# Performance work log

Hardware: AMD Instinct MI355X
Metric: run time of the kernel (lower is better)

Reference implementation:

```python
import jax, jax.numpy as jnp
import numpy as np

HEADS = 16
DIM_HEAD = 64
NONCAUSAL_ATTN_LEN = 64


def setup_inputs() -> dict:
    key = jax.random.key(0)
    k1, k2, k3 = jax.random.split(key, 3)
    b, n, d = 2, 2048, 1024
    inner = HEADS * DIM_HEAD
    x = jax.random.normal(k1, (b, n, d), dtype=jnp.float32)
    mask = jnp.ones((b, n), dtype=bool)
    w_qkv = jax.random.normal(k2, (d, 3 * inner), dtype=jnp.float32) * 0.02
    w_out = jax.random.normal(k3, (inner, d), dtype=jnp.float32) * 0.02
    b_out = jnp.zeros((d,), dtype=jnp.float32)
    return {"x": x, "mask": mask, "w_qkv": w_qkv, "w_out": w_out, "b_out": b_out}


def reference(x, mask, w_qkv, w_out, b_out):
    b, n, _ = x.shape
    h, dh = HEADS, DIM_HEAD
    scale = dh ** -0.5
    qkv = x @ w_qkv                                  # [b, n, 3*h*dh]
    q, k, v = jnp.split(qkv, 3, axis=-1)
    # 'b n (h d) -> b h n d'
    reshape = lambda t: t.reshape(b, n, h, dh).transpose(0, 2, 1, 3)
    q, k, v = reshape(q), reshape(k), reshape(v)
    dots = jnp.einsum('bhid,bhjd->bhij', q, k) * scale  # [b,h,n,n]
    neg = -jnp.finfo(dots.dtype).max
    # padding mask: attend only where both query and key positions are valid
    pm = mask[:, None, :, None] & mask[:, None, None, :]
    dots = jnp.where(~pm, neg, dots)
    # causal mask (strict upper triangle), with noncausal prefix block unmasked
    cm = jnp.triu(jnp.ones((n, n), dtype=bool), k=1)
    L = NONCAUSAL_ATTN_LEN
    if L > 1:
        cm = cm.at[:L, :L].set(False)
    dots = jnp.where(cm, neg, dots)
    attn = jax.nn.softmax(dots, axis=-1)
    out = jnp.einsum('bhij,bhjd->bhid', attn, v)     # [b,h,n,dh]
    out = out.transpose(0, 2, 1, 3).reshape(b, n, h * dh)  # 'b h n d -> b n (h d)'
    return out @ w_out + b_out
```

## Files before the change

### kernel.cpp

```cpp
#include <hip/hip_runtime.h>

typedef __bf16 bf16x8 __attribute__((ext_vector_type(8)));
typedef __bf16 bf16x4 __attribute__((ext_vector_type(4)));
typedef float  f32x4  __attribute__((ext_vector_type(4)));

#define SC2 0.18033688011112042f

__device__ __forceinline__ void gload16(const void* g, void* l) {
    __builtin_amdgcn_global_load_lds(
        (const __attribute__((address_space(1))) unsigned int*)g,
        (__attribute__((address_space(3))) unsigned int*)l, 16, 0, 0);
}

__global__ __launch_bounds__(256) void cast_f32_bf16_k(
    const float* __restrict__ in, __bf16* __restrict__ out, int n4)
{
    int i = blockIdx.x * blockDim.x + threadIdx.x;
    if (i < n4) {
        float4 v = ((const float4*)in)[i];
        bf16x4 o;
        o[0] = (__bf16)v.x; o[1] = (__bf16)v.y; o[2] = (__bf16)v.z; o[3] = (__bf16)v.w;
        ((bf16x4*)out)[i] = o;
    }
}

__global__ __launch_bounds__(1024) void transpose_cast_k(
    const float* __restrict__ in, __bf16* __restrict__ out, int R, int C)
{
    __shared__ float tile[32][33];
    int c0 = blockIdx.x * 32, r0 = blockIdx.y * 32;
    int tx = threadIdx.x, ty = threadIdx.y;
    tile[ty][tx] = in[(size_t)(r0 + ty) * C + (c0 + tx)];
    __syncthreads();
    out[(size_t)(c0 + ty) * R + (r0 + tx)] = (__bf16)tile[tx][ty];
}

template<int MODE>
__global__ __launch_bounds__(256) void gemm_bf16_k(
    const __bf16* __restrict__ A, const __bf16* __restrict__ Bt,
    void* __restrict__ Cout, const float* __restrict__ bias,
    int M, int N, int K)
{
    __shared__ __bf16 As[128 * 32];
    __shared__ __bf16 Bs[128 * 32];
    const int tid = threadIdx.x;
    const int m0 = blockIdx.x * 128, n0 = blockIdx.y * 128;
    const int wave = tid >> 6, lane = tid & 63;
    const int lr = lane & 15, lk = lane >> 4;

    const int row4 = lane >> 2;
    const int sg   = (lane & 3) ^ (row4 & 3);

    const int wm = (wave >> 1) * 64, wn = (wave & 1) * 64;

    f32x4 acc[4][4] = {};

    for (int k0 = 0; k0 < K; k0 += 32) {
#pragma unroll
        for (int c = 0; c < 2; ++c) {
            int row = c * 64 + wave * 16 + row4;
            gload16(A  + (size_t)(m0 + row) * K + k0 + sg * 8,
                    (char*)As + c * 4096 + wave * 1024);
            gload16(Bt + (size_t)(n0 + row) * K + k0 + sg * 8,
                    (char*)Bs + c * 4096 + wave * 1024);
        }
        __syncthreads();

        bf16x8 af[4], bfr[4];
#pragma unroll
        for (int i = 0; i < 4; ++i) {
            int row = wm + i * 16 + lr;
            af[i]  = *(const bf16x8*)((char*)As + row * 64 + ((lk ^ (row & 3)) << 4));
        }
#pragma unroll
        for (int j = 0; j < 4; ++j) {
            int row = wn + j * 16 + lr;
            bfr[j] = *(const bf16x8*)((char*)Bs + row * 64 + ((lk ^ (row & 3)) << 4));
        }
        __builtin_amdgcn_s_setprio(1);
#pragma unroll
        for (int i = 0; i < 4; ++i)
#pragma unroll
            for (int j = 0; j < 4; ++j)
                acc[i][j] = __builtin_amdgcn_mfma_f32_16x16x32_bf16(
                    af[i], bfr[j], acc[i][j], 0, 0, 0);
        __builtin_amdgcn_s_setprio(0);
        __syncthreads();
    }

#pragma unroll
    for (int i = 0; i < 4; ++i) {
#pragma unroll
        for (int j = 0; j < 4; ++j) {
            int row0 = m0 + wm + i * 16 + lk * 4;
            int col  = n0 + wn + j * 16 + lr;
            if (MODE == 0) {
                int which = col >> 10, rem = col & 1023;
                int h = rem >> 6, dh = rem & 63;
                int bb = row0 >> 11, nn0 = row0 & 2047;
                if (which == 2) {
                    bf16x4 o;
#pragma unroll
                    for (int r = 0; r < 4; ++r) o[r] = (__bf16)acc[i][j][r];
                    size_t off = (size_t)8388608 +
                                 (((size_t)bb * 16 + h) * 64 + dh) * 2048 + nn0;
                    *(bf16x4*)((__bf16*)Cout + off) = o;
                } else {
#pragma unroll
                    for (int r = 0; r < 4; ++r) {
                        size_t off = ((((size_t)which * 2 + bb) * 16 + h) * 2048
                                      + nn0 + r) * 64 + dh;
                        ((__bf16*)Cout)[off] = (__bf16)acc[i][j][r];
                    }
                }
            } else {
#pragma unroll
                for (int r = 0; r < 4; ++r)
                    ((float*)Cout)[(size_t)(row0 + r) * N + col] =
                        acc[i][j][r] + bias[col];
            }
        }
    }
}

__global__ __launch_bounds__(256) void flash_attn_k(
    const __bf16* __restrict__ qkv, __bf16* __restrict__ out)
{
    __shared__ __bf16 Ks[2][64 * 64];
    __shared__ __bf16 Vt[2][64 * 64];
    __shared__ __bf16 Ps[4 * 16 * 64];

    const int tid = threadIdx.x;
    const int g = blockIdx.x;
    const int xcd = g & 7, i = g >> 3;
    const int bh = xcd + 8 * (i & 3);
    const int qt = 31 - (i >> 2);
    const int b = bh >> 4, h = bh & 15;
    const int wave = tid >> 6, lane = tid & 63;
    const int lr = lane & 15, lk = lane >> 4;

    const size_t headoff = ((size_t)b * 16 + h) * 2048 * 64;
    const __bf16* Qp  = qkv + headoff;
    const __bf16* Kp  = qkv + (size_t)4194304 + headoff;
    const __bf16* Vtp = qkv + (size_t)8388608 + headoff;

    const int row8 = lane >> 3;
    const int sg   = (lane & 7) ^ row8;

    bf16x8 qf[2];
    {
        const __bf16* qa = Qp + (size_t)(qt * 64 + wave * 16 + lr) * 64 + lk * 8;
        qf[0] = *(const bf16x8*)(qa);
        qf[1] = *(const bf16x8*)(qa + 32);
    }

    float m = -1e30f, l = 0.f;
    f32x4 acc_o[4] = {};

    char* PsW = (char*)Ps + wave * 2048;

    auto stage = [&](int t, int bufi) {
        const int j0 = t * 64;
#pragma unroll
        for (int c = 0; c < 2; ++c) {
            int row = c * 32 + wave * 8 + row8;
            gload16(Kp + (size_t)(j0 + row) * 64 + sg * 8,
                    (char*)&Ks[bufi][0] + c * 4096 + wave * 1024);
            gload16(Vtp + (size_t)row * 2048 + j0 + sg * 8,
                    (char*)&Vt[bufi][0] + c * 4096 + wave * 1024);
        }
    };

    auto process = [&](int bufi, bool diag) {
        f32x4 sacc[4] = {};
        __builtin_amdgcn_s_setprio(1);
#pragma unroll
        for (int nf = 0; nf < 4; ++nf) {
            int arow = nf * 16 + lr;
#pragma unroll
            for (int ks = 0; ks < 2; ++ks) {
                int kb = (arow * 128 + (ks * 32 + lk * 8) * 2) ^ ((arow & 7) << 4);
                bf16x8 kf = *(const bf16x8*)((char*)&Ks[bufi][0] + kb);
                sacc[nf] = __builtin_amdgcn_mfma_f32_16x16x32_bf16(
                    kf, qf[ks], sacc[nf], 0, 0, 0);
            }
        }
        __builtin_amdgcn_s_setprio(0);
        if (diag) {
#pragma unroll
            for (int nf = 0; nf < 4; ++nf)
#pragma unroll
                for (int r = 0; r < 4; ++r)
                    if (nf * 16 + lk * 4 + r > wave * 16 + lr)
                        sacc[nf][r] = -1e30f;
        }
        float v = sacc[0][0];
#pragma unroll
        for (int nf = 0; nf < 4; ++nf)
#pragma unroll
            for (int r = 0; r < 4; ++r) v = fmaxf(v, sacc[nf][r]);
        v = fmaxf(v, __shfl_xor(v, 16));
        v = fmaxf(v, __shfl_xor(v, 32));
        float alpha = 1.f;
        bool resc = __any(v - m > 8.f);
        if (resc) {
            float mnew = fmaxf(m, v);
            alpha = exp2f((m - mnew) * SC2);
            m = mnew;
        }
        float rsum = 0.f;
#pragma unroll
        for (int nf = 0; nf < 4; ++nf) {
            bf16x4 o;
#pragma unroll
            for (int r = 0; r < 4; ++r) {
                float p = exp2f((sacc[nf][r] - m) * SC2);
                rsum += p;
                o[r] = (__bf16)p;
            }
            int pb = (lr * 128 + nf * 32 + lk * 8) ^ ((lr & 7) << 4);
            *(bf16x4*)(PsW + pb) = o;
        }
        rsum += __shfl_xor(rsum, 16);
        rsum += __shfl_xor(rsum, 32);
        l = l * alpha + rsum;
        if (resc) {
            float a_r[4];
#pragma unroll
            for (int r = 0; r < 4; ++r) a_r[r] = __shfl(alpha, lk * 4 + r);
#pragma unroll
            for (int nf = 0; nf < 4; ++nf)
#pragma unroll
                for (int r = 0; r < 4; ++r) acc_o[nf][r] *= a_r[r];
        }
        __builtin_amdgcn_s_setprio(1);
#pragma unroll
        for (int ks = 0; ks < 2; ++ks) {
            int pb = (lr * 128 + ks * 64 + lk * 16) ^ ((lr & 7) << 4);
            bf16x8 pa = *(const bf16x8*)(PsW + pb);
#pragma unroll
            for (int nf = 0; nf < 4; ++nf) {
                int d = nf * 16 + lr;
                int vb = (d * 128 + ks * 64 + lk * 16) ^ ((d & 7) << 4);
                bf16x8 vf = *(const bf16x8*)((char*)&Vt[bufi][0] + vb);
                acc_o[nf] = __builtin_amdgcn_mfma_f32_16x16x32_bf16(
                    pa, vf, acc_o[nf], 0, 0, 0);
            }
        }
        __builtin_amdgcn_s_setprio(0);
    };

    const int nt = qt + 1;
    stage(0, 0);
    for (int t = 0; t < nt; ++t) {
        __syncthreads();
        if (t + 1 < nt) stage(t + 1, (t + 1) & 1);
        process(t & 1, t == qt && qt > 0);
    }

    float l_row[4];
#pragma unroll
    for (int r = 0; r < 4; ++r) l_row[r] = __shfl(l, lk * 4 + r);
    const int rowbase = (b << 11) + qt * 64 + wave * 16 + lk * 4;
    const int colbase = h * 64 + lr;
#pragma unroll
    for (int nf = 0; nf < 4; ++nf)
#pragma unroll
        for (int r = 0; r < 4; ++r)
            out[(size_t)(rowbase + r) * 1024 + colbase + nf * 16] =
                (__bf16)(acc_o[nf][r] / l_row[r]);
}

extern "C" void kernel_launch(void* const* d_in, const int* in_sizes, int n_in,
                              void* d_out, int out_size, void* d_ws, size_t ws_size,
                              hipStream_t stream)
{
    const float* x     = (const float*)d_in[0];
    const float* w_qkv = (const float*)d_in[2];
    const float* w_out = (const float*)d_in[3];
    const float* b_out = (const float*)d_in[4];

    char* ws = (char*)d_ws;
    __bf16* xb    = (__bf16*)(ws);
    __bf16* wqkvT = (__bf16*)(ws + 8388608);
    __bf16* woutT = (__bf16*)(ws + 14680064);
    __bf16* qkvp  = (__bf16*)(ws + 16777216);
    __bf16* aout  = (__bf16*)(ws + 41943040);

    cast_f32_bf16_k<<<4096, 256, 0, stream>>>(x, xb, 1048576);
    transpose_cast_k<<<dim3(96, 32), dim3(32, 32), 0, stream>>>(w_qkv, wqkvT, 1024, 3072);
    transpose_cast_k<<<dim3(32, 32), dim3(32, 32), 0, stream>>>(w_out, woutT, 1024, 1024);

    gemm_bf16_k<0><<<dim3(32, 24), 256, 0, stream>>>(xb, wqkvT, (void*)qkvp, nullptr,
                                                     4096, 3072, 1024);
    flash_attn_k<<<1024, 256, 0, stream>>>(qkvp, aout);
    gemm_bf16_k<1><<<dim3(32, 8), 256, 0, stream>>>(aout, woutT, (void*)d_out, b_out,
                                                    4096, 1024, 1024);
}
```

Measured before the change: 125.8 us.

## Load K/V fragments directly from global memory instead of double-buffered LDS staging

Drops the shared-memory double buffers for K and V and the per-tile __syncthreads. Each wave now reads its MFMA operands straight from global memory, relying on L1/L2 to serve the redundant reads across the four waves. It also sets a launch-bounds occupancy hint of 6, rewrites the max reduction as a tree, and replaces the final division with a reciprocal multiply. The cost is higher global and L2 traffic, with each wave reading K/V separately and using strided V loads, plus exposed load latency now that there is no explicit prefetch.

```diff
diff --git a/kernel.cpp b/kernel.cpp
--- a/kernel.cpp
+++ b/kernel.cpp
@@ -123,29 +123,23 @@
     }
 }
 
-__global__ __launch_bounds__(256) void flash_attn_k(
+__global__ __launch_bounds__(256, 6) void flash_attn_k(
     const __bf16* __restrict__ qkv, __bf16* __restrict__ out)
 {
-    __shared__ __bf16 Ks[2][64 * 64];
-    __shared__ __bf16 Vt[2][64 * 64];
     __shared__ __bf16 Ps[4 * 16 * 64];
 
-    const int tid = threadIdx.x;
     const int g = blockIdx.x;
     const int xcd = g & 7, i = g >> 3;
     const int bh = xcd + 8 * (i & 3);
     const int qt = 31 - (i >> 2);
     const int b = bh >> 4, h = bh & 15;
-    const int wave = tid >> 6, lane = tid & 63;
+    const int wave = threadIdx.x >> 6, lane = threadIdx.x & 63;
     const int lr = lane & 15, lk = lane >> 4;
 
     const size_t headoff = ((size_t)b * 16 + h) * 2048 * 64;
     const __bf16* Qp  = qkv + headoff;
     const __bf16* Kp  = qkv + (size_t)4194304 + headoff;
     const __bf16* Vtp = qkv + (size_t)8388608 + headoff;
-
-    const int row8 = lane >> 3;
-    const int sg   = (lane & 7) ^ row8;
 
     bf16x8 qf[2];
     {
@@ -158,35 +152,28 @@
     f32x4 acc_o[4] = {};
 
     char* PsW = (char*)Ps + wave * 2048;
-
-    auto stage = [&](int t, int bufi) {
+    const __bf16* Kl = Kp  + lr * 64 + lk * 8;
+    const __bf16* Vl = Vtp + lr * 2048 + lk * 8;
+
+    for (int t = 0; t <= qt; ++t) {
         const int j0 = t * 64;
-#pragma unroll
-        for (int c = 0; c < 2; ++c) {
-            int row = c * 32 + wave * 8 + row8;
-            gload16(Kp + (size_t)(j0 + row) * 64 + sg * 8,
-                    (char*)&Ks[bufi][0] + c * 4096 + wave * 1024);
-            gload16(Vtp + (size_t)row * 2048 + j0 + sg * 8,
-                    (char*)&Vt[bufi][0] + c * 4096 + wave * 1024);
-        }
-    };
-
-    auto process = [&](int bufi, bool diag) {
+        const __bf16* Kt = Kl + j0 * 64;
+        const __bf16* Vt = Vl + j0;
+
         f32x4 sacc[4] = {};
         __builtin_amdgcn_s_setprio(1);
 #pragma unroll
         for (int nf = 0; nf < 4; ++nf) {
-            int arow = nf * 16 + lr;
 #pragma unroll
             for (int ks = 0; ks < 2; ++ks) {
-                int kb = (arow * 128 + (ks * 32 + lk * 8) * 2) ^ ((arow & 7) << 4);
-                bf16x8 kf = *(const bf16x8*)((char*)&Ks[bufi][0] + kb);
+                bf16x8 kf = *(const bf16x8*)(Kt + nf * 1024 + ks * 32);
                 sacc[nf] = __builtin_amdgcn_mfma_f32_16x16x32_bf16(
                     kf, qf[ks], sacc[nf], 0, 0, 0);
             }
         }
         __builtin_amdgcn_s_setprio(0);
-        if (diag) {
+
+        if (t == qt && qt > 0) {
 #pragma unroll
             for (int nf = 0; nf < 4; ++nf)
 #pragma unroll
@@ -194,13 +181,15 @@
                     if (nf * 16 + lk * 4 + r > wave * 16 + lr)
                         sacc[nf][r] = -1e30f;
         }
-        float v = sacc[0][0];
-#pragma unroll
-        for (int nf = 0; nf < 4; ++nf)
-#pragma unroll
-            for (int r = 0; r < 4; ++r) v = fmaxf(v, sacc[nf][r]);
+
+        float v = fmaxf(fmaxf(fmaxf(sacc[0][0], sacc[0][1]), fmaxf(sacc[0][2], sacc[0][3])),
+                        fmaxf(fmaxf(sacc[1][0], sacc[1][1]), fmaxf(sacc[1][2], sacc[1][3])));
+        float v2 = fmaxf(fmaxf(fmaxf(sacc[2][0], sacc[2][1]), fmaxf(sacc[2][2], sacc[2][3])),
+                         fmaxf(fmaxf(sacc[3][0], sacc[3][1]), fmaxf(sacc[3][2], sacc[3][3])));
+        v = fmaxf(v, v2);
         v = fmaxf(v, __shfl_xor(v, 16));
         v = fmaxf(v, __shfl_xor(v, 32));
+
         float alpha = 1.f;
         bool resc = __any(v - m > 8.f);
         if (resc) {
@@ -208,6 +197,7 @@
             alpha = exp2f((m - mnew) * SC2);
             m = mnew;
         }
+
         float rsum = 0.f;
 #pragma unroll
         for (int nf = 0; nf < 4; ++nf) {
@@ -233,6 +223,7 @@
 #pragma unroll
                 for (int r = 0; r < 4; ++r) acc_o[nf][r] *= a_r[r];
         }
+
         __builtin_amdgcn_s_setprio(1);
 #pragma unroll
         for (int ks = 0; ks < 2; ++ks) {
@@ -240,27 +231,17 @@
             bf16x8 pa = *(const bf16x8*)(PsW + pb);
 #pragma unroll
             for (int nf = 0; nf < 4; ++nf) {
-                int d = nf * 16 + lr;
-                int vb = (d * 128 + ks * 64 + lk * 16) ^ ((d & 7) << 4);
-                bf16x8 vf = *(const bf16x8*)((char*)&Vt[bufi][0] + vb);
+                bf16x8 vf = *(const bf16x8*)(Vt + nf * 32768 + ks * 32);
                 acc_o[nf] = __builtin_amdgcn_mfma_f32_16x16x32_bf16(
                     pa, vf, acc_o[nf], 0, 0, 0);
             }
         }
         __builtin_amdgcn_s_setprio(0);
-    };
-
-    const int nt = qt + 1;
-    stage(0, 0);
-    for (int t = 0; t < nt; ++t) {
-        __syncthreads();
-        if (t + 1 < nt) stage(t + 1, (t + 1) & 1);
-        process(t & 1, t == qt && qt > 0);
     }
 
     float l_row[4];
 #pragma unroll
-    for (int r = 0; r < 4; ++r) l_row[r] = __shfl(l, lk * 4 + r);
+    for (int r = 0; r < 4; ++r) l_row[r] = 1.f / __shfl(l, lk * 4 + r);
     const int rowbase = (b << 11) + qt * 64 + wave * 16 + lk * 4;
     const int colbase = h * 64 + lr;
 #pragma unroll
@@ -268,7 +249,7 @@
 #pragma unroll
         for (int r = 0; r < 4; ++r)
             out[(size_t)(rowbase + r) * 1024 + colbase + nf * 16] =
-                (__bf16)(acc_o[nf][r] / l_row[r]);
+                (__bf16)(acc_o[nf][r] * l_row[r]);
 }
 
 extern "C" void kernel_launch(void* const* d_in, const int* in_sizes, int n_in,
```

After: 223.7 us. +77.9%, slower.

## Pair causal query tiles per block and fold softmax scale into Q

Applied to the files above, without the earlier changes.

Each attention block now handles two query tiles, qt and 31-qt, from the same head. They share every staged K/V tile, which evens out causal work across blocks and halves the grid to 512. The QKV GEMM epilogue pre-multiplies Q by scale*log2(e), so the softmax exp2 no longer needs a multiply, and the final normalization uses a reciprocal instead of a divide. In exchange it holds two sets of Q fragments and accumulators, which raises register pressure, and Q is rounded to bf16 after scaling.

```diff
diff --git a/kernel.cpp b/kernel.cpp
--- a/kernel.cpp
+++ b/kernel.cpp
@@ -106,11 +106,12 @@
                                  (((size_t)bb * 16 + h) * 64 + dh) * 2048 + nn0;
                     *(bf16x4*)((__bf16*)Cout + off) = o;
                 } else {
+                    float sc = (which == 0) ? SC2 : 1.f;
 #pragma unroll
                     for (int r = 0; r < 4; ++r) {
                         size_t off = ((((size_t)which * 2 + bb) * 16 + h) * 2048
                                       + nn0 + r) * 64 + dh;
-                        ((__bf16*)Cout)[off] = (__bf16)acc[i][j][r];
+                        ((__bf16*)Cout)[off] = (__bf16)(acc[i][j][r] * sc);
                     }
                 }
             } else {
@@ -130,13 +131,13 @@
     __shared__ __bf16 Vt[2][64 * 64];
     __shared__ __bf16 Ps[4 * 16 * 64];
 
-    const int tid = threadIdx.x;
     const int g = blockIdx.x;
     const int xcd = g & 7, i = g >> 3;
     const int bh = xcd + 8 * (i & 3);
-    const int qt = 31 - (i >> 2);
+    const int qp = i >> 2;
+    const int qtA = qp, qtB = 31 - qp;
     const int b = bh >> 4, h = bh & 15;
-    const int wave = tid >> 6, lane = tid & 63;
+    const int wave = threadIdx.x >> 6, lane = threadIdx.x & 63;
     const int lr = lane & 15, lk = lane >> 4;
 
     const size_t headoff = ((size_t)b * 16 + h) * 2048 * 64;
@@ -147,15 +148,18 @@
     const int row8 = lane >> 3;
     const int sg   = (lane & 7) ^ row8;
 
-    bf16x8 qf[2];
+    bf16x8 qfA[2], qfB[2];
     {
-        const __bf16* qa = Qp + (size_t)(qt * 64 + wave * 16 + lr) * 64 + lk * 8;
-        qf[0] = *(const bf16x8*)(qa);
-        qf[1] = *(const bf16x8*)(qa + 32);
-    }
-
-    float m = -1e30f, l = 0.f;
-    f32x4 acc_o[4] = {};
+        const __bf16* qa = Qp + (size_t)(qtA * 64 + wave * 16 + lr) * 64 + lk * 8;
+        qfA[0] = *(const bf16x8*)(qa);
+        qfA[1] = *(const bf16x8*)(qa + 32);
+        const __bf16* qb = Qp + (size_t)(qtB * 64 + wave * 16 + lr) * 64 + lk * 8;
+        qfB[0] = *(const bf16x8*)(qb);
+        qfB[1] = *(const bf16x8*)(qb + 32);
+    }
+
+    float mA = -1e30f, lA = 0.f, mB = -1e30f, lB = 0.f;
+    f32x4 oA[4] = {}, oB[4] = {};
 
     char* PsW = (char*)Ps + wave * 2048;
 
@@ -171,7 +175,8 @@
         }
     };
 
-    auto process = [&](int bufi, bool diag) {
+    auto process = [&](int bufi, const bf16x8 (&qf)[2], float& m, float& l,
+                       f32x4 (&acc_o)[4], bool diag) {
         f32x4 sacc[4] = {};
         __builtin_amdgcn_s_setprio(1);
 #pragma unroll
@@ -194,18 +199,18 @@
                     if (nf * 16 + lk * 4 + r > wave * 16 + lr)
                         sacc[nf][r] = -1e30f;
         }
-        float v = sacc[0][0];
-#pragma unroll
-        for (int nf = 0; nf < 4; ++nf)
-#pragma unroll
-            for (int r = 0; r < 4; ++r) v = fmaxf(v, sacc[nf][r]);
+        float v = fmaxf(fmaxf(fmaxf(sacc[0][0], sacc[0][1]), fmaxf(sacc[0][2], sacc[0][3])),
+                        fmaxf(fmaxf(sacc[1][0], sacc[1][1]), fmaxf(sacc[1][2], sacc[1][3])));
+        float v2 = fmaxf(fmaxf(fmaxf(sacc[2][0], sacc[2][1]), fmaxf(sacc[2][2], sacc[2][3])),
+                         fmaxf(fmaxf(sacc[3][0], sacc[3][1]), fmaxf(sacc[3][2], sacc[3][3])));
+        v = fmaxf(v, v2);
         v = fmaxf(v, __shfl_xor(v, 16));
         v = fmaxf(v, __shfl_xor(v, 32));
         float alpha = 1.f;
         bool resc = __any(v - m > 8.f);
         if (resc) {
             float mnew = fmaxf(m, v);
-            alpha = exp2f((m - mnew) * SC2);
+            alpha = exp2f(m - mnew);
             m = mnew;
         }
         float rsum = 0.f;
@@ -214,7 +219,7 @@
             bf16x4 o;
 #pragma unroll
             for (int r = 0; r < 4; ++r) {
-                float p = exp2f((sacc[nf][r] - m) * SC2);
+                float p = exp2f(sacc[nf][r] - m);
                 rsum += p;
                 o[r] = (__bf16)p;
             }
@@ -250,25 +255,32 @@
         __builtin_amdgcn_s_setprio(0);
     };
 
-    const int nt = qt + 1;
+    const int nt = qtB + 1;
     stage(0, 0);
     for (int t = 0; t < nt; ++t) {
         __syncthreads();
         if (t + 1 < nt) stage(t + 1, (t + 1) & 1);
-        process(t & 1, t == qt && qt > 0);
-    }
-
-    float l_row[4];
-#pragma unroll
-    for (int r = 0; r < 4; ++r) l_row[r] = __shfl(l, lk * 4 + r);
-    const int rowbase = (b << 11) + qt * 64 + wave * 16 + lk * 4;
+        if (t <= qtA) process(t & 1, qfA, mA, lA, oA, t == qtA && qtA > 0);
+        process(t & 1, qfB, mB, lB, oB, t == qtB);
+    }
+
+    float lAr[4], lBr[4];
+#pragma unroll
+    for (int r = 0; r < 4; ++r) {
+        lAr[r] = 1.f / __shfl(lA, lk * 4 + r);
+        lBr[r] = 1.f / __shfl(lB, lk * 4 + r);
+    }
+    const int rowbase = (b << 11) + wave * 16 + lk * 4;
     const int colbase = h * 64 + lr;
 #pragma unroll
     for (int nf = 0; nf < 4; ++nf)
 #pragma unroll
-        for (int r = 0; r < 4; ++r)
-            out[(size_t)(rowbase + r) * 1024 + colbase + nf * 16] =
-                (__bf16)(acc_o[nf][r] / l_row[r]);
+        for (int r = 0; r < 4; ++r) {
+            out[(size_t)(rowbase + qtA * 64 + r) * 1024 + colbase + nf * 16] =
+                (__bf16)(oA[nf][r] * lAr[r]);
+            out[(size_t)(rowbase + qtB * 64 + r) * 1024 + colbase + nf * 16] =
+                (__bf16)(oB[nf][r] * lBr[r]);
+        }
 }
 
 extern "C" void kernel_launch(void* const* d_in, const int* in_sizes, int n_in,
@@ -293,7 +305,7 @@
 
     gemm_bf16_k<0><<<dim3(32, 24), 256, 0, stream>>>(xb, wqkvT, (void*)qkvp, nullptr,
                                                      4096, 3072, 1024);
-    flash_attn_k<<<1024, 256, 0, stream>>>(qkvp, aout);
+    flash_attn_k<<<512, 256, 0, stream>>>(qkvp, aout);
     gemm_bf16_k<1><<<dim3(32, 8), 256, 0, stream>>>(aout, woutT, (void*)d_out, b_out,
                                                     4096, 1024, 1024);
 }
```

New measurement: 125.9 us. No clear change (+0.1%).
